# Optimization experiments

Measured on AMD Instinct MI355X. Metric: run time of the kernel, lower is better.

## Reference

```python
import jax, jax.numpy as jnp
import numpy as np

N, D, H, E = 4096, 512, 8, 131072
DH = D // H
BN_EPS = 1e-5


def setup_inputs() -> dict:
    key = jax.random.key(0)
    ks = jax.random.split(key, 12)
    def w(k, shape):
        return jax.random.normal(k, shape, dtype=jnp.float32) * 0.02
    return {
        'x': jax.random.normal(ks[0], (N, D), dtype=jnp.float32),
        'edge_index': jax.random.randint(ks[1], (2, E), 0, N),
        'edge_attr': jax.random.normal(ks[2], (E, D), dtype=jnp.float32),
        # GINE MLP: Linear(D,D) -> ReLU -> Linear(D,D)  (torch layout [out,in])
        'w_gin1': w(ks[3], (D, D)), 'b_gin1': jnp.zeros((D,), jnp.float32),
        'w_gin2': w(ks[4], (D, D)), 'b_gin2': jnp.zeros((D,), jnp.float32),
        # MultiheadAttention in/out projections
        'w_qkv': w(ks[5], (3 * D, D)), 'b_qkv': jnp.zeros((3 * D,), jnp.float32),
        'w_o': w(ks[6], (D, D)), 'b_o': jnp.zeros((D,), jnp.float32),
        # BatchNorm affine params
        'bn1l_g': jnp.ones((D,), jnp.float32), 'bn1l_b': jnp.zeros((D,), jnp.float32),
        'bn1a_g': jnp.ones((D,), jnp.float32), 'bn1a_b': jnp.zeros((D,), jnp.float32),
        # FFN: D -> 2D -> D
        'w_ff1': w(ks[7], (2 * D, D)), 'b_ff1': jnp.zeros((2 * D,), jnp.float32),
        'w_ff2': w(ks[8], (D, 2 * D)), 'b_ff2': jnp.zeros((D,), jnp.float32),
        'bn2_g': jnp.ones((D,), jnp.float32), 'bn2_b': jnp.zeros((D,), jnp.float32),
    }


def _bn(x, g, b):
    # BatchNorm1d in training mode: batch statistics over the node dim
    m = jnp.mean(x, axis=0)
    v = jnp.var(x, axis=0)
    return (x - m) * jax.lax.rsqrt(v + BN_EPS) * g + b


def _forward(x, edge_index, edge_attr,
             w_gin1, b_gin1, w_gin2, b_gin2,
             w_qkv, b_qkv, w_o, b_o,
             bn1l_g, bn1l_b, bn1a_g, bn1a_b,
             w_ff1, b_ff1, w_ff2, b_ff2, bn2_g, bn2_b):
    h_in = x
    src, dst = edge_index[0], edge_index[1]
    # --- local GINEConv: nn((1+eps)*x + sum_j relu(x_j + e_ji)), eps=0 ---
    msg = jax.nn.relu(x[src] + edge_attr)                       # [E, D]
    agg = jax.ops.segment_sum(msg, dst, num_segments=N)         # [N, D]
    gin_h = x + agg
    h_local = jax.nn.relu(gin_h @ w_gin1.T + b_gin1) @ w_gin2.T + b_gin2
    h_local = _bn(h_in + h_local, bn1l_g, bn1l_b)               # residual + BN
    # --- global multi-head self-attention over all nodes (single graph) ---
    qkv = x @ w_qkv.T + b_qkv                                   # [N, 3D]
    q, k, v = jnp.split(qkv, 3, axis=-1)
    q = q.reshape(N, H, DH).transpose(1, 0, 2)                  # [H, N, DH]
    k = k.reshape(N, H, DH).transpose(1, 0, 2)
    v = v.reshape(N, H, DH).transpose(1, 0, 2)
    scores = jnp.einsum('hnd,hmd->hnm', q, k) / np.float32(np.sqrt(DH))
    attn = jax.nn.softmax(scores, axis=-1)                      # [H, N, N]
    o = jnp.einsum('hnm,hmd->hnd', attn, v).transpose(1, 0, 2).reshape(N, D)
    h_attn = _bn(h_in + (o @ w_o.T + b_o), bn1a_g, bn1a_b)
    # --- combine branches + FFN block ---
    h = h_local + h_attn
    h = h + (jax.nn.relu(h @ w_ff1.T + b_ff1) @ w_ff2.T + b_ff2)
    return _bn(h, bn2_g, bn2_b)


def reference(x, edge_index, edge_attr,
              w_gin1, b_gin1, w_gin2, b_gin2,
              w_qkv, b_qkv, w_o, b_o,
              bn1l_g, bn1l_b, bn1a_g, bn1a_b,
              w_ff1, b_ff1, w_ff2, b_ff2, bn2_g, bn2_b):
    return _forward(x, edge_index, edge_attr,
                    w_gin1, b_gin1, w_gin2, b_gin2,
                    w_qkv, b_qkv, w_o, b_o,
                    bn1l_g, bn1l_b, bn1a_g, bn1a_b,
                    w_ff1, b_ff1, w_ff2, b_ff2, bn2_g, bn2_b)
```

## Files before the change

### kernel.cpp

```cpp
#include <hip/hip_runtime.h>

#define Nn 4096
#define Dd 512
#define Hh 8
#define Ee 131072
#define DEGCAP 96

typedef __attribute__((ext_vector_type(8))) short short8v;
typedef __attribute__((ext_vector_type(8))) unsigned short ushort8v;
typedef __attribute__((ext_vector_type(4))) short short4v;
typedef __attribute__((ext_vector_type(4))) float f32x4v;
typedef __attribute__((ext_vector_type(4))) unsigned short ushort4v;

__device__ __forceinline__ float bf2f(unsigned short u) {
    return __uint_as_float(((unsigned int)u) << 16);
}
__device__ __forceinline__ unsigned short f2bf(float f) {
    unsigned int u = __float_as_uint(f);
    return (unsigned short)((u + 0x7fff + ((u >> 16) & 1)) >> 16);
}
__device__ __forceinline__ void gl_lds16(const void* g, void* l) {
    __builtin_amdgcn_global_load_lds((const __attribute__((address_space(1))) void*)g,
                                     (__attribute__((address_space(3))) void*)l, 16, 0, 0);
}

struct CastJobs {
    const float* src[6];
    unsigned short* dst[6];
    int start[7];
    int* cnt;
    float* stats;
};

__global__ __launch_bounds__(256) void cast_multi(CastJobs cj) {
    int gid = blockIdx.x * 256 + threadIdx.x;
    if (gid < 4096) cj.cnt[gid] = 0;
    if (gid < 6144) cj.stats[gid] = 0.f;
    int b = blockIdx.x;
    int j = 0;
    while (b >= cj.start[j + 1]) j++;
    int off = (b - cj.start[j]) * 1024 + threadIdx.x * 4;
    f32x4v v = *(const f32x4v*)(cj.src[j] + off);
    ushort4v o;
    o.x = f2bf(v.x); o.y = f2bf(v.y); o.z = f2bf(v.z); o.w = f2bf(v.w);
    *(ushort4v*)(cj.dst[j] + off) = o;
}

__global__ __launch_bounds__(256) void edge_scatter(const int* __restrict__ ei,
                                                    int* __restrict__ cnt,
                                                    int* __restrict__ eidx) {
    int e = blockIdx.x * 256 + threadIdx.x;
    int d = ei[Ee + e];
    int pos = atomicAdd(&cnt[d], 1);
    if (pos < DEGCAP) eidx[d * DEGCAP + pos] = e;
}

__global__ __launch_bounds__(256) void gine_gather(const float* __restrict__ x,
                                                   const int* __restrict__ ei,
                                                   const float* __restrict__ ea,
                                                   const int* __restrict__ cnt,
                                                   const int* __restrict__ eidx,
                                                   unsigned short* __restrict__ gh,
                                                   unsigned short* __restrict__ xb) {
    __shared__ int se[DEGCAP];
    __shared__ int ss[DEGCAP];
    __shared__ float part[512];
    const int node = blockIdx.x;
    const int t = threadIdx.x;
    const int deg = min(cnt[node], DEGCAP);
    const int tc = t & 127, ep = t >> 7;

    if (t < deg) {
        int e = eidx[node * DEGCAP + t];
        se[t] = e;
        ss[t] = ei[e];
    }
    __syncthreads();

    f32x4v acc = {0.f, 0.f, 0.f, 0.f};
    int k = ep;
    while (k + 2 < deg) {
        int e0 = se[k], s0 = ss[k];
        int e1 = se[k + 2], s1 = ss[k + 2];
        f32x4v ev0 = *(const f32x4v*)(ea + (size_t)e0 * Dd + tc * 4);
        f32x4v xv0 = *(const f32x4v*)(x + (size_t)s0 * Dd + tc * 4);
        f32x4v ev1 = *(const f32x4v*)(ea + (size_t)e1 * Dd + tc * 4);
        f32x4v xv1 = *(const f32x4v*)(x + (size_t)s1 * Dd + tc * 4);
#pragma unroll
        for (int i = 0; i < 4; i++) {
            acc[i] += fmaxf(xv0[i] + ev0[i], 0.f);
            acc[i] += fmaxf(xv1[i] + ev1[i], 0.f);
        }
        k += 4;
    }
    if (k < deg) {
        int e0 = se[k], s0 = ss[k];
        f32x4v ev0 = *(const f32x4v*)(ea + (size_t)e0 * Dd + tc * 4);
        f32x4v xv0 = *(const f32x4v*)(x + (size_t)s0 * Dd + tc * 4);
#pragma unroll
        for (int i = 0; i < 4; i++) acc[i] += fmaxf(xv0[i] + ev0[i], 0.f);
    }

    if (ep) *(f32x4v*)&part[tc * 4] = acc;
    __syncthreads();
    if (!ep) {
        f32x4v o = *(const f32x4v*)&part[tc * 4];
        f32x4v xd = *(const f32x4v*)(x + (size_t)node * Dd + tc * 4);
        ushort4v ov, xv;
#pragma unroll
        for (int i = 0; i < 4; i++) {
            ov[i] = f2bf(xd[i] + acc[i] + o[i]);
            xv[i] = f2bf(xd[i]);
        }
        *(ushort4v*)(gh + (size_t)node * Dd + tc * 4) = ov;
        *(ushort4v*)(xb + (size_t)node * Dd + tc * 4) = xv;
    }
}

template <int K, int MB, bool RELU, bool OUTBF16, bool ADDRES, bool SXADD, int SOFF, bool ACOMB>
__device__ __forceinline__ void gemm_body(char* smem,
                                          const short* __restrict__ A,
                                          const short* __restrict__ B,
                                          const float* __restrict__ bias,
                                          const float* __restrict__ res,
                                          void* __restrict__ outp, int Nc,
                                          const float* __restrict__ sx,
                                          float* __restrict__ stats,
                                          const unsigned short* __restrict__ op0,
                                          const unsigned short* __restrict__ op1,
                                          const float* __restrict__ lsum,
                                          int bx, int by, int t) {
    constexpr int BM = MB * 32;
    short* lA = (short*)smem;
    short* lB = (short*)(smem + MB * 2048);
    float* sst = (float*)(smem + MB * 2048 + 8192);
    const int lane = t & 63, w = t >> 6;
    const int wr = w >> 1, wc = w & 1;
    const int l15 = lane & 15, lhi = lane >> 4;
    const int m0 = by * BM, n0 = bx * 128;
    f32x4v acc[MB][4] = {};
    const int c0 = t, c1 = t + 256;

    for (int k0 = 0; k0 < K; k0 += 32) {
        __syncthreads();
        if constexpr (ACOMB) {
            int r = c0 >> 2, s = c0 & 3;
            int row = m0 + r;
            int kb = k0 + s * 8;
            int h = k0 >> 6;
            float inv = 1.f / (lsum[(size_t)h * Nn + row] + lsum[(size_t)(Hh + h) * Nn + row]);
            ushort8v p0 = *(const ushort8v*)&op0[(size_t)row * 512 + kb];
            ushort8v p1 = *(const ushort8v*)&op1[(size_t)row * 512 + kb];
            short8v ov;
#pragma unroll
            for (int i = 0; i < 8; i++) ov[i] = (short)f2bf((bf2f(p0[i]) + bf2f(p1[i])) * inv);
            *(short8v*)((char*)lA + c0 * 16) = ov;
        } else {
            gl_lds16(A + (size_t)(m0 + (c0 >> 2)) * K + k0 + (c0 & 3) * 8, (char*)lA + c0 * 16);
            if constexpr (MB == 4)
                gl_lds16(A + (size_t)(m0 + (c1 >> 2)) * K + k0 + (c1 & 3) * 8, (char*)lA + c1 * 16);
        }
        gl_lds16(B + (size_t)(n0 + (c0 >> 2)) * K + k0 + (c0 & 3) * 8, (char*)lB + c0 * 16);
        gl_lds16(B + (size_t)(n0 + (c1 >> 2)) * K + k0 + (c1 & 3) * 8, (char*)lB + c1 * 16);
        __syncthreads();
        short8v af[MB], bf[4];
#pragma unroll
        for (int m = 0; m < MB; m++)
            af[m] = *(const short8v*)&lA[(wr * (MB * 16) + m * 16 + l15) * 32 + lhi * 8];
#pragma unroll
        for (int n = 0; n < 4; n++)
            bf[n] = *(const short8v*)&lB[(wc * 64 + n * 16 + l15) * 32 + lhi * 8];
#pragma unroll
        for (int m = 0; m < MB; m++)
#pragma unroll
            for (int n = 0; n < 4; n++)
                acc[m][n] = __builtin_amdgcn_mfma_f32_16x16x32_bf16(af[m], bf[n], acc[m][n], 0, 0, 0);
    }

    float csum[4] = {0.f, 0.f, 0.f, 0.f}, cssq[4] = {0.f, 0.f, 0.f, 0.f};

#pragma unroll
    for (int m = 0; m < MB; m++)
#pragma unroll
        for (int n = 0; n < 4; n++)
#pragma unroll
            for (int j = 0; j < 4; j++) {
                int col = n0 + wc * 64 + n * 16 + l15;
                int row = m0 + wr * (MB * 16) + m * 16 + lhi * 4 + j;
                size_t idx = (size_t)row * Nc + col;
                float v = acc[m][n][j] + bias[col];
                if (RELU) v = fmaxf(v, 0.f);
                if (ADDRES) v += res[idx];
                if constexpr (SOFF >= 0) {
                    float a = SXADD ? (sx[idx] + v) : v;
                    csum[n] += a;
                    cssq[n] += a * a;
                }
                if (OUTBF16)
                    ((unsigned short*)outp)[idx] = f2bf(v);
                else
                    ((float*)outp)[idx] = v;
            }

    if constexpr (SOFF >= 0) {
        sst[t] = 0.f;
        __syncthreads();
#pragma unroll
        for (int n = 0; n < 4; n++) {
            float s = csum[n], q = cssq[n];
            s += __shfl_xor(s, 16); s += __shfl_xor(s, 32);
            q += __shfl_xor(q, 16); q += __shfl_xor(q, 32);
            if (lhi == 0) {
                int c = wc * 64 + n * 16 + l15;
                atomicAdd(&sst[c * 2], s);
                atomicAdd(&sst[c * 2 + 1], q);
            }
        }
        __syncthreads();
        atomicAdd(&stats[SOFF + (t & 1) * 512 + n0 + (t >> 1)], sst[t]);
    }
}

__device__ __forceinline__ void attn_body(char* smem, const short* __restrict__ qkv,
                                          unsigned short* __restrict__ opart0,
                                          unsigned short* __restrict__ opart1,
                                          float* __restrict__ lsum,
                                          int bx, int by, int t) {
    const int lane = t & 63, w = t >> 6;
    const int h = by >> 1, half = by & 1;
    const int kvbase = half * 2048;
    const int qw = bx * 128 + w * 32;
    const int l15 = lane & 15, lhi = lane >> 4;
    const int ksw = l15 & 7;
    const int qs3 = (l15 >> 1) & 7;
    unsigned short* __restrict__ opart = half ? opart1 : opart0;

    short* pP = (short*)(smem + 32768) + w * 2048;

    short8v qf[2][2];
#pragma unroll
    for (int g = 0; g < 2; g++)
#pragma unroll
        for (int kk = 0; kk < 2; kk++)
            qf[g][kk] = *(const short8v*)&qkv[(size_t)(qw + g * 16 + l15) * 1536 + h * 64 + kk * 32 + lhi * 8];

    f32x4v oacc[2][4] = {};
    float lrow[2] = {0.f, 0.f};
    const float SC2 = 0.125f * 1.44269504f;

    int kidx[4][2];
#pragma unroll
    for (int r = 0; r < 4; r++)
#pragma unroll
        for (int kk = 0; kk < 2; kk++)
            kidx[r][kk] = (l15 + r * 16) * 64 + (((kk * 4 + lhi) ^ ksw) * 8);

    int pw_idx[4], prd_idx[2];
#pragma unroll
    for (int c2 = 0; c2 < 4; c2++)
        pw_idx[c2] = l15 * 64 + (((c2 * 2 + (lhi >> 1)) ^ qs3) * 8) + ((lhi & 1) * 4);
#pragma unroll
    for (int c = 0; c < 2; c++)
        prd_idx[c] = l15 * 64 + (((c * 4 + lhi) ^ qs3) * 8);

    unsigned vbase0 = (unsigned)(size_t)(smem + 16384) + lhi * 256 + l15 * 2;

    auto stage = [&](int kt, int b) {
        int kv0 = kvbase + kt * 64;
#pragma unroll
        for (int i = 0; i < 2; i++) {
            gl_lds16(qkv + (size_t)(kv0 + (t >> 3) + 32 * i) * 1536 + 512 + h * 64 + ((t & 7) ^ ((t >> 3) & 7)) * 8,
                     smem + b * 8192 + t * 16 + i * 4096);
        }
#pragma unroll
        for (int i = 0; i < 2; i++) {
            int db = (t >> 7) + 2 * i;
            int kv = (t >> 1) & 63;
            int dh_in = (t & 1) * 8;
            gl_lds16(qkv + (size_t)(kv0 + kv) * 1536 + 1024 + h * 64 + db * 16 + dh_in,
                     smem + 16384 + b * 8192 + t * 16 + i * 4096);
        }
    };

    stage(0, 0);
    __syncthreads();

    for (int kt = 0; kt < 32; kt++) {
        const int b = kt & 1;
        if (kt + 1 < 32) stage(kt + 1, b ^ 1);

        const short* Kb = (const short*)smem + b * 4096;
        const unsigned vbase = vbase0 + b * 8192;

        f32x4v s0[4] = {}, s1[4] = {};
        __builtin_amdgcn_s_setprio(1);
#pragma unroll
        for (int r = 0; r < 4; r++) {
            short8v k0 = *(const short8v*)&Kb[kidx[r][0]];
            short8v k1 = *(const short8v*)&Kb[kidx[r][1]];
            s0[r] = __builtin_amdgcn_mfma_f32_16x16x32_bf16(k0, qf[0][0], s0[r], 0, 0, 0);
            s0[r] = __builtin_amdgcn_mfma_f32_16x16x32_bf16(k1, qf[0][1], s0[r], 0, 0, 0);
            s1[r] = __builtin_amdgcn_mfma_f32_16x16x32_bf16(k0, qf[1][0], s1[r], 0, 0, 0);
            s1[r] = __builtin_amdgcn_mfma_f32_16x16x32_bf16(k1, qf[1][1], s1[r], 0, 0, 0);
        }
        __builtin_amdgcn_s_setprio(0);

#pragma unroll
        for (int g = 0; g < 2; g++) {
            f32x4v* s = g ? s1 : s0;
            float p[16];
            float rs = 0.f;
#pragma unroll
            for (int r = 0; r < 4; r++)
#pragma unroll
                for (int j = 0; j < 4; j++) {
                    float e = exp2f(fmaf(s[r][j], SC2, -4.f));
                    p[r * 4 + j] = e;
                    rs += e;
                }
            rs += __shfl_xor(rs, 16);
            rs += __shfl_xor(rs, 32);
            lrow[g] += rs;

            short* pPg = pP + g * 1024;
#pragma unroll
            for (int c2 = 0; c2 < 4; c2++) {
                short4v pk;
#pragma unroll
                for (int j = 0; j < 4; j++) pk[j] = (short)f2bf(p[c2 * 4 + j]);
                *(short4v*)&pPg[pw_idx[c2]] = pk;
            }
        }
        asm volatile("" ::: "memory");

        short8v pf[2][2];
#pragma unroll
        for (int g = 0; g < 2; g++)
#pragma unroll
            for (int c = 0; c < 2; c++)
                pf[g][c] = *(const short8v*)&pP[g * 1024 + prd_idx[c]];

        short4v v00a, v00b, v01a, v01b, v10a, v10b, v11a, v11b;
        short4v v20a, v20b, v21a, v21b, v30a, v30b, v31a, v31b;
        asm volatile("ds_read_b64_tr_b16 %0, %1" : "=v"(v00a) : "v"(vbase));
        asm volatile("ds_read_b64_tr_b16 %0, %1 offset:128" : "=v"(v00b) : "v"(vbase));
        asm volatile("ds_read_b64_tr_b16 %0, %1 offset:1024" : "=v"(v01a) : "v"(vbase));
        asm volatile("ds_read_b64_tr_b16 %0, %1 offset:1152" : "=v"(v01b) : "v"(vbase));
        asm volatile("ds_read_b64_tr_b16 %0, %1 offset:2048" : "=v"(v10a) : "v"(vbase));
        asm volatile("ds_read_b64_tr_b16 %0, %1 offset:2176" : "=v"(v10b) : "v"(vbase));
        asm volatile("ds_read_b64_tr_b16 %0, %1 offset:3072" : "=v"(v11a) : "v"(vbase));
        asm volatile("ds_read_b64_tr_b16 %0, %1 offset:3200" : "=v"(v11b) : "v"(vbase));
        asm volatile("ds_read_b64_tr_b16 %0, %1 offset:4096" : "=v"(v20a) : "v"(vbase));
        asm volatile("ds_read_b64_tr_b16 %0, %1 offset:4224" : "=v"(v20b) : "v"(vbase));
        asm volatile("ds_read_b64_tr_b16 %0, %1 offset:5120" : "=v"(v21a) : "v"(vbase));
        asm volatile("ds_read_b64_tr_b16 %0, %1 offset:5248" : "=v"(v21b) : "v"(vbase));
        asm volatile("ds_read_b64_tr_b16 %0, %1 offset:6144" : "=v"(v30a) : "v"(vbase));
        asm volatile("ds_read_b64_tr_b16 %0, %1 offset:6272" : "=v"(v30b) : "v"(vbase));
        asm volatile("ds_read_b64_tr_b16 %0, %1 offset:7168" : "=v"(v31a) : "v"(vbase));
        asm volatile("ds_read_b64_tr_b16 %0, %1 offset:7296" : "=v"(v31b) : "v"(vbase));

        asm volatile("s_waitcnt lgkmcnt(0)" ::: "memory");
        __builtin_amdgcn_sched_barrier(0);

#define VFCAT(a, b) __builtin_shufflevector(a, b, 0, 1, 2, 3, 4, 5, 6, 7)
        short8v vv[4][2];
        vv[0][0] = VFCAT(v00a, v00b); vv[0][1] = VFCAT(v01a, v01b);
        vv[1][0] = VFCAT(v10a, v10b); vv[1][1] = VFCAT(v11a, v11b);
        vv[2][0] = VFCAT(v20a, v20b); vv[2][1] = VFCAT(v21a, v21b);
        vv[3][0] = VFCAT(v30a, v30b); vv[3][1] = VFCAT(v31a, v31b);
#undef VFCAT
        __builtin_amdgcn_s_setprio(1);
#pragma unroll
        for (int g = 0; g < 2; g++)
#pragma unroll
            for (int n = 0; n < 4; n++) {
                oacc[g][n] = __builtin_amdgcn_mfma_f32_16x16x32_bf16(pf[g][0], vv[n][0], oacc[g][n], 0, 0, 0);
                oacc[g][n] = __builtin_amdgcn_mfma_f32_16x16x32_bf16(pf[g][1], vv[n][1], oacc[g][n], 0, 0, 0);
            }
        __builtin_amdgcn_s_setprio(0);

        __syncthreads();
    }

#pragma unroll
    for (int g = 0; g < 2; g++) {
#pragma unroll
        for (int j = 0; j < 4; j++) {
            int row = qw + g * 16 + lhi * 4 + j;
#pragma unroll
            for (int n = 0; n < 4; n++)
                opart[(size_t)row * Dd + h * 64 + n * 16 + l15] = f2bf(oacc[g][n][j]);
        }
        if (lhi == 0)
            lsum[(size_t)(half * Hh + h) * Nn + qw + g * 16 + l15] = lrow[g];
    }
}

__global__ __launch_bounds__(256) void gin1_qkv(const short* ginh, const short* wg1b,
                                                const float* b_gin1, unsigned short* t1,
                                                const short* xb, const short* wqkvb,
                                                const float* b_qkv, unsigned short* qkvb) {
    __shared__ char smem[16384];
    int b = blockIdx.x, t = threadIdx.x;
    if (b < 256) {
        gemm_body<512, 2, true, true, false, false, -1, false>(
            smem, ginh, wg1b, b_gin1, nullptr, t1, 512, nullptr, nullptr,
            nullptr, nullptr, nullptr, b & 3, b >> 2, t);
    } else {
        int bb = b - 256;
        gemm_body<512, 4, false, true, false, false, -1, false>(
            smem, xb, wqkvb, b_qkv, nullptr, qkvb, 1536, nullptr, nullptr,
            nullptr, nullptr, nullptr, bb % 12, bb / 12, t);
    }
}

__global__ __launch_bounds__(256) void gin2_attn(const short* qkvb, unsigned short* op0,
                                                 unsigned short* op1, float* lsum,
                                                 const short* t1, const short* wg2b,
                                                 const float* b_gin2, float* hlp,
                                                 const float* x, float* stats) {
    __shared__ char smem[49152];
    int b = blockIdx.x, t = threadIdx.x;
    if (b < 512) {
        attn_body(smem, qkvb, op0, op1, lsum, b & 31, b >> 5, t);
    } else {
        int bb = b - 512;
        gemm_body<512, 2, false, false, false, true, 0, false>(
            smem, t1, wg2b, b_gin2, nullptr, hlp, 512, x, stats,
            nullptr, nullptr, nullptr, bb & 3, bb >> 2, t);
    }
}

__global__ __launch_bounds__(256) void oproj_fused(const short* wob, const float* b_o,
                                                   float* attn_pre, const float* x, float* stats,
                                                   const unsigned short* op0,
                                                   const unsigned short* op1,
                                                   const float* lsum) {
    __shared__ char smem[13312];
    gemm_body<512, 2, false, false, false, true, 1024, true>(
        smem, nullptr, wob, b_o, nullptr, attn_pre, 512, x, stats,
        op0, op1, lsum, blockIdx.x, blockIdx.y, threadIdx.x);
}

__global__ __launch_bounds__(256) void ff1_k(const short* hb, const short* wf1b,
                                             const float* b_ff1, unsigned short* t2) {
    __shared__ char smem[16384];
    gemm_body<512, 4, true, true, false, false, -1, false>(
        smem, hb, wf1b, b_ff1, nullptr, t2, 1024, nullptr, nullptr,
        nullptr, nullptr, nullptr, blockIdx.x, blockIdx.y, threadIdx.x);
}

__global__ __launch_bounds__(256) void ff2_k(const short* t2, const short* wf2b,
                                             const float* b_ff2, const float* hbuf,
                                             float* dout, float* stats) {
    __shared__ char smem[13312];
    gemm_body<1024, 2, false, false, true, false, 4096, false>(
        smem, t2, wf2b, b_ff2, hbuf, dout, 512, nullptr, stats,
        nullptr, nullptr, nullptr, blockIdx.x, blockIdx.y, threadIdx.x);
}

__global__ __launch_bounds__(256) void bn_combine(const float* __restrict__ x,
                                                  const float* __restrict__ p1,
                                                  const float* __restrict__ p2,
                                                  const float* __restrict__ stats,
                                                  const float* __restrict__ g1,
                                                  const float* __restrict__ b1,
                                                  const float* __restrict__ g2,
                                                  const float* __restrict__ b2,
                                                  float* __restrict__ h,
                                                  unsigned short* __restrict__ hb) {
    int i0 = (blockIdx.x * 256 + threadIdx.x) * 4;
    int c0 = i0 & 511;
    f32x4v xv = *(const f32x4v*)(x + i0);
    f32x4v av = *(const f32x4v*)(p1 + i0);
    f32x4v bv = *(const f32x4v*)(p2 + i0);
    f32x4v hv;
    ushort4v hbv;
#pragma unroll
    for (int e = 0; e < 4; e++) {
        int c = c0 + e;
        float ma = stats[c] * (1.f / Nn);
        float va = stats[512 + c] * (1.f / Nn) - ma * ma;
        float sA = g1[c] * rsqrtf(va + 1e-5f);
        float bA = b1[c] - ma * sA;
        float mb = stats[1024 + c] * (1.f / Nn);
        float vb = stats[1536 + c] * (1.f / Nn) - mb * mb;
        float sB = g2[c] * rsqrtf(vb + 1e-5f);
        float bB = b2[c] - mb * sB;
        float a = xv[e] + av[e];
        float b = xv[e] + bv[e];
        float val = a * sA + bA + b * sB + bB;
        hv[e] = val;
        hbv[e] = f2bf(val);
    }
    *(f32x4v*)(h + i0) = hv;
    *(ushort4v*)(hb + i0) = hbv;
}

__global__ __launch_bounds__(256) void bn_apply(float* __restrict__ out,
                                                const float* __restrict__ stats,
                                                const float* __restrict__ g,
                                                const float* __restrict__ b) {
    int i0 = (blockIdx.x * 256 + threadIdx.x) * 4;
    int c0 = i0 & 511;
    f32x4v v = *(const f32x4v*)(out + i0);
#pragma unroll
    for (int e = 0; e < 4; e++) {
        int c = c0 + e;
        float m = stats[4096 + c] * (1.f / Nn);
        float va = stats[4608 + c] * (1.f / Nn) - m * m;
        float s = g[c] * rsqrtf(va + 1e-5f);
        v[e] = (v[e] - m) * s + b[c];
    }
    *(f32x4v*)(out + i0) = v;
}

extern "C" void kernel_launch(void* const* d_in, const int* in_sizes, int n_in,
                              void* d_out, int out_size, void* d_ws, size_t ws_size,
                              hipStream_t stream) {
    const float* x = (const float*)d_in[0];
    const int* ei = (const int*)d_in[1];
    const float* ea = (const float*)d_in[2];
    const float* w_gin1 = (const float*)d_in[3];
    const float* b_gin1 = (const float*)d_in[4];
    const float* w_gin2 = (const float*)d_in[5];
    const float* b_gin2 = (const float*)d_in[6];
    const float* w_qkv = (const float*)d_in[7];
    const float* b_qkv = (const float*)d_in[8];
    const float* w_o = (const float*)d_in[9];
    const float* b_o = (const float*)d_in[10];
    const float* bn1l_g = (const float*)d_in[11];
    const float* bn1l_b = (const float*)d_in[12];
    const float* bn1a_g = (const float*)d_in[13];
    const float* bn1a_b = (const float*)d_in[14];
    const float* w_ff1 = (const float*)d_in[15];
    const float* b_ff1 = (const float*)d_in[16];
    const float* w_ff2 = (const float*)d_in[17];
    const float* b_ff2 = (const float*)d_in[18];
    const float* bn2_g = (const float*)d_in[19];
    const float* bn2_b = (const float*)d_in[20];

    char* ws = (char*)d_ws;
    unsigned short* wg1b = (unsigned short*)(ws + 0);
    unsigned short* wg2b = (unsigned short*)(ws + 524288);
    unsigned short* wqkvb = (unsigned short*)(ws + 1048576);
    unsigned short* wob = (unsigned short*)(ws + 2621440);
    unsigned short* wf1b = (unsigned short*)(ws + 3145728);
    unsigned short* wf2b = (unsigned short*)(ws + 4194304);
    unsigned short* xb = (unsigned short*)(ws + 5242880);
    unsigned short* qkvb = (unsigned short*)(ws + 9437184);
    int* eidx = (int*)(ws + 22020096);
    int* cnt = (int*)(ws + 23592960);
    unsigned short* ginh = (unsigned short*)(ws + 30408704);
    float* lsum = (float*)(ws + 30408704);
    unsigned short* t1 = (unsigned short*)(ws + 34603008);
    float* hlp = (float*)(ws + 38797312);
    float* attn_pre = (float*)(ws + 51380224);
    float* hbuf = (float*)(ws + 59768832);
    unsigned short* opart0 = (unsigned short*)(ws + 59768832);
    unsigned short* hb = (unsigned short*)(ws + 68157440);
    unsigned short* t2 = (unsigned short*)(ws + 72351744);
    unsigned short* opart1 = (unsigned short*)(ws + 72351744);
    float* stats = (float*)(ws + 80740352);

    CastJobs cj;
    cj.src[0] = w_gin1; cj.dst[0] = wg1b;
    cj.src[1] = w_gin2; cj.dst[1] = wg2b;
    cj.src[2] = w_qkv;  cj.dst[2] = wqkvb;
    cj.src[3] = w_o;    cj.dst[3] = wob;
    cj.src[4] = w_ff1;  cj.dst[4] = wf1b;
    cj.src[5] = w_ff2;  cj.dst[5] = wf2b;
    cj.cnt = cnt;
    cj.stats = stats;
    int nelem[6] = {Dd * Dd, Dd * Dd, 3 * Dd * Dd, Dd * Dd, 2 * Dd * Dd, 2 * Dd * Dd};
    cj.start[0] = 0;
    for (int i = 0; i < 6; i++) cj.start[i + 1] = cj.start[i] + nelem[i] / 1024;
    cast_multi<<<cj.start[6], 256, 0, stream>>>(cj);

    edge_scatter<<<Ee / 256, 256, 0, stream>>>(ei, cnt, eidx);
    gine_gather<<<Nn, 256, 0, stream>>>(x, ei, ea, cnt, eidx, ginh, xb);

    gin1_qkv<<<640, 256, 0, stream>>>((const short*)ginh, (const short*)wg1b, b_gin1, t1,
                                      (const short*)xb, (const short*)wqkvb, b_qkv, qkvb);

    gin2_attn<<<768, 256, 0, stream>>>((const short*)qkvb, opart0, opart1, lsum,
                                       (const short*)t1, (const short*)wg2b, b_gin2, hlp,
                                       x, stats);

    oproj_fused<<<dim3(4, 64), 256, 0, stream>>>((const short*)wob, b_o, attn_pre, x, stats,
                                                 opart0, opart1, lsum);

    bn_combine<<<Nn * Dd / 1024, 256, 0, stream>>>(x, hlp, attn_pre, stats,
                                                   bn1l_g, bn1l_b, bn1a_g, bn1a_b, hbuf, hb);

    ff1_k<<<dim3(8, 32), 256, 0, stream>>>((const short*)hb, (const short*)wf1b, b_ff1, t2);
    ff2_k<<<dim3(4, 64), 256, 0, stream>>>((const short*)t2, (const short*)wf2b, b_ff2,
                                           hbuf, (float*)d_out, stats);

    bn_apply<<<Nn * Dd / 1024, 256, 0, stream>>>((float*)d_out, stats, bn2_g, bn2_b);
}
```

Measured before the change: 260.6 us.

## Split attention KV into quarters with 64 queries per wave; use bf16 FFN residual

The attention work is reorganised: each block now covers 256 queries (64 per wave) against one quarter of the keys, so every K/V tile loaded into shared memory is reused by twice as many queries. Four partial outputs and four partial row sums are combined in the o-projection prologue, and shared memory grows to 64KB with launch bounds of two blocks per CU. Separately, bn_combine no longer writes an fp32 copy of h, and ff2 adds the bf16 hb as its residual, cutting memory traffic at a small precision cost. The larger per-wave register state for the accumulators may reduce occupancy or cause spills.

```diff
diff --git a/kernel.cpp b/kernel.cpp
--- a/kernel.cpp
+++ b/kernel.cpp
@@ -117,17 +117,19 @@
     }
 }
 
-template <int K, int MB, bool RELU, bool OUTBF16, bool ADDRES, bool SXADD, int SOFF, bool ACOMB>
+template <int K, int MB, bool RELU, bool OUTBF16, int RESMODE, bool SXADD, int SOFF, bool ACOMB>
 __device__ __forceinline__ void gemm_body(char* smem,
                                           const short* __restrict__ A,
                                           const short* __restrict__ B,
                                           const float* __restrict__ bias,
-                                          const float* __restrict__ res,
+                                          const void* __restrict__ res,
                                           void* __restrict__ outp, int Nc,
                                           const float* __restrict__ sx,
                                           float* __restrict__ stats,
                                           const unsigned short* __restrict__ op0,
                                           const unsigned short* __restrict__ op1,
+                                          const unsigned short* __restrict__ op2,
+                                          const unsigned short* __restrict__ op3,
                                           const float* __restrict__ lsum,
                                           int bx, int by, int t) {
     constexpr int BM = MB * 32;
@@ -148,12 +150,16 @@
             int row = m0 + r;
             int kb = k0 + s * 8;
             int h = k0 >> 6;
-            float inv = 1.f / (lsum[(size_t)h * Nn + row] + lsum[(size_t)(Hh + h) * Nn + row]);
+            float inv = 1.f / (lsum[(size_t)h * Nn + row] + lsum[(size_t)(Hh + h) * Nn + row] +
+                               lsum[(size_t)(2 * Hh + h) * Nn + row] + lsum[(size_t)(3 * Hh + h) * Nn + row]);
             ushort8v p0 = *(const ushort8v*)&op0[(size_t)row * 512 + kb];
             ushort8v p1 = *(const ushort8v*)&op1[(size_t)row * 512 + kb];
+            ushort8v p2 = *(const ushort8v*)&op2[(size_t)row * 512 + kb];
+            ushort8v p3 = *(const ushort8v*)&op3[(size_t)row * 512 + kb];
             short8v ov;
 #pragma unroll
-            for (int i = 0; i < 8; i++) ov[i] = (short)f2bf((bf2f(p0[i]) + bf2f(p1[i])) * inv);
+            for (int i = 0; i < 8; i++)
+                ov[i] = (short)f2bf((bf2f(p0[i]) + bf2f(p1[i]) + bf2f(p2[i]) + bf2f(p3[i])) * inv);
             *(short8v*)((char*)lA + c0 * 16) = ov;
         } else {
             gl_lds16(A + (size_t)(m0 + (c0 >> 2)) * K + k0 + (c0 & 3) * 8, (char*)lA + c0 * 16);
@@ -190,7 +196,8 @@
                 size_t idx = (size_t)row * Nc + col;
                 float v = acc[m][n][j] + bias[col];
                 if (RELU) v = fmaxf(v, 0.f);
-                if (ADDRES) v += res[idx];
+                if constexpr (RESMODE == 1) v += ((const float*)res)[idx];
+                if constexpr (RESMODE == 2) v += bf2f(((const unsigned short*)res)[idx]);
                 if constexpr (SOFF >= 0) {
                     float a = SXADD ? (sx[idx] + v) : v;
                     csum[n] += a;
@@ -222,30 +229,32 @@
 }
 
 __device__ __forceinline__ void attn_body(char* smem, const short* __restrict__ qkv,
-                                          unsigned short* __restrict__ opart0,
-                                          unsigned short* __restrict__ opart1,
+                                          unsigned short* __restrict__ op0,
+                                          unsigned short* __restrict__ op1,
+                                          unsigned short* __restrict__ op2,
+                                          unsigned short* __restrict__ op3,
                                           float* __restrict__ lsum,
                                           int bx, int by, int t) {
     const int lane = t & 63, w = t >> 6;
-    const int h = by >> 1, half = by & 1;
-    const int kvbase = half * 2048;
-    const int qw = bx * 128 + w * 32;
+    const int h = by >> 2, quarter = by & 3;
+    const int kvbase = quarter * 1024;
+    const int qw = bx * 256 + w * 64;
     const int l15 = lane & 15, lhi = lane >> 4;
     const int ksw = l15 & 7;
     const int qs3 = (l15 >> 1) & 7;
-    unsigned short* __restrict__ opart = half ? opart1 : opart0;
-
-    short* pP = (short*)(smem + 32768) + w * 2048;
-
-    short8v qf[2][2];
-#pragma unroll
-    for (int g = 0; g < 2; g++)
+    unsigned short* __restrict__ opart = quarter == 0 ? op0 : quarter == 1 ? op1 : quarter == 2 ? op2 : op3;
+
+    short* pP = (short*)(smem + 32768) + w * 4096;
+
+    short8v qf[4][2];
+#pragma unroll
+    for (int g = 0; g < 4; g++)
 #pragma unroll
         for (int kk = 0; kk < 2; kk++)
             qf[g][kk] = *(const short8v*)&qkv[(size_t)(qw + g * 16 + l15) * 1536 + h * 64 + kk * 32 + lhi * 8];
 
-    f32x4v oacc[2][4] = {};
-    float lrow[2] = {0.f, 0.f};
+    f32x4v oacc[4][4] = {};
+    float lrow[4] = {0.f, 0.f, 0.f, 0.f};
     const float SC2 = 0.125f * 1.44269504f;
 
     int kidx[4][2];
@@ -285,36 +294,36 @@
     stage(0, 0);
     __syncthreads();
 
-    for (int kt = 0; kt < 32; kt++) {
+    for (int kt = 0; kt < 16; kt++) {
         const int b = kt & 1;
-        if (kt + 1 < 32) stage(kt + 1, b ^ 1);
+        if (kt + 1 < 16) stage(kt + 1, b ^ 1);
 
         const short* Kb = (const short*)smem + b * 4096;
         const unsigned vbase = vbase0 + b * 8192;
 
-        f32x4v s0[4] = {}, s1[4] = {};
+        f32x4v s[4][4] = {};
         __builtin_amdgcn_s_setprio(1);
 #pragma unroll
         for (int r = 0; r < 4; r++) {
             short8v k0 = *(const short8v*)&Kb[kidx[r][0]];
             short8v k1 = *(const short8v*)&Kb[kidx[r][1]];
-            s0[r] = __builtin_amdgcn_mfma_f32_16x16x32_bf16(k0, qf[0][0], s0[r], 0, 0, 0);
-            s0[r] = __builtin_amdgcn_mfma_f32_16x16x32_bf16(k1, qf[0][1], s0[r], 0, 0, 0);
-            s1[r] = __builtin_amdgcn_mfma_f32_16x16x32_bf16(k0, qf[1][0], s1[r], 0, 0, 0);
-            s1[r] = __builtin_amdgcn_mfma_f32_16x16x32_bf16(k1, qf[1][1], s1[r], 0, 0, 0);
+#pragma unroll
+            for (int g = 0; g < 4; g++) {
+                s[g][r] = __builtin_amdgcn_mfma_f32_16x16x32_bf16(k0, qf[g][0], s[g][r], 0, 0, 0);
+                s[g][r] = __builtin_amdgcn_mfma_f32_16x16x32_bf16(k1, qf[g][1], s[g][r], 0, 0, 0);
+            }
         }
         __builtin_amdgcn_s_setprio(0);
 
 #pragma unroll
-        for (int g = 0; g < 2; g++) {
-            f32x4v* s = g ? s1 : s0;
+        for (int g = 0; g < 4; g++) {
             float p[16];
             float rs = 0.f;
 #pragma unroll
             for (int r = 0; r < 4; r++)
 #pragma unroll
                 for (int j = 0; j < 4; j++) {
-                    float e = exp2f(fmaf(s[r][j], SC2, -4.f));
+                    float e = exp2f(fmaf(s[g][r][j], SC2, -4.f));
                     p[r * 4 + j] = e;
                     rs += e;
                 }
@@ -333,9 +342,9 @@
         }
         asm volatile("" ::: "memory");
 
-        short8v pf[2][2];
-#pragma unroll
-        for (int g = 0; g < 2; g++)
+        short8v pf[4][2];
+#pragma unroll
+        for (int g = 0; g < 4; g++)
 #pragma unroll
             for (int c = 0; c < 2; c++)
                 pf[g][c] = *(const short8v*)&pP[g * 1024 + prd_idx[c]];
@@ -371,7 +380,7 @@
 #undef VFCAT
         __builtin_amdgcn_s_setprio(1);
 #pragma unroll
-        for (int g = 0; g < 2; g++)
+        for (int g = 0; g < 4; g++)
 #pragma unroll
             for (int n = 0; n < 4; n++) {
                 oacc[g][n] = __builtin_amdgcn_mfma_f32_16x16x32_bf16(pf[g][0], vv[n][0], oacc[g][n], 0, 0, 0);
@@ -383,7 +392,7 @@
     }
 
 #pragma unroll
-    for (int g = 0; g < 2; g++) {
+    for (int g = 0; g < 4; g++) {
 #pragma unroll
         for (int j = 0; j < 4; j++) {
             int row = qw + g * 16 + lhi * 4 + j;
@@ -392,7 +401,7 @@
                 opart[(size_t)row * Dd + h * 64 + n * 16 + l15] = f2bf(oacc[g][n][j]);
         }
         if (lhi == 0)
-            lsum[(size_t)(half * Hh + h) * Nn + qw + g * 16 + l15] = lrow[g];
+            lsum[(size_t)(quarter * Hh + h) * Nn + qw + g * 16 + l15] = lrow[g];
     }
 }
 
@@ -403,31 +412,32 @@
     __shared__ char smem[16384];
     int b = blockIdx.x, t = threadIdx.x;
     if (b < 256) {
-        gemm_body<512, 2, true, true, false, false, -1, false>(
+        gemm_body<512, 2, true, true, 0, false, -1, false>(
             smem, ginh, wg1b, b_gin1, nullptr, t1, 512, nullptr, nullptr,
-            nullptr, nullptr, nullptr, b & 3, b >> 2, t);
+            nullptr, nullptr, nullptr, nullptr, nullptr, b & 3, b >> 2, t);
     } else {
         int bb = b - 256;
-        gemm_body<512, 4, false, true, false, false, -1, false>(
+        gemm_body<512, 4, false, true, 0, false, -1, false>(
             smem, xb, wqkvb, b_qkv, nullptr, qkvb, 1536, nullptr, nullptr,
-            nullptr, nullptr, nullptr, bb % 12, bb / 12, t);
-    }
-}
-
-__global__ __launch_bounds__(256) void gin2_attn(const short* qkvb, unsigned short* op0,
-                                                 unsigned short* op1, float* lsum,
-                                                 const short* t1, const short* wg2b,
-                                                 const float* b_gin2, float* hlp,
-                                                 const float* x, float* stats) {
-    __shared__ char smem[49152];
+            nullptr, nullptr, nullptr, nullptr, nullptr, bb % 12, bb / 12, t);
+    }
+}
+
+__global__ __launch_bounds__(256, 2) void gin2_attn(const short* qkvb, unsigned short* op0,
+                                                    unsigned short* op1, unsigned short* op2,
+                                                    unsigned short* op3, float* lsum,
+                                                    const short* t1, const short* wg2b,
+                                                    const float* b_gin2, float* hlp,
+                                                    const float* x, float* stats) {
+    __shared__ char smem[65536];
     int b = blockIdx.x, t = threadIdx.x;
     if (b < 512) {
-        attn_body(smem, qkvb, op0, op1, lsum, b & 31, b >> 5, t);
+        attn_body(smem, qkvb, op0, op1, op2, op3, lsum, b & 15, b >> 4, t);
     } else {
         int bb = b - 512;
-        gemm_body<512, 2, false, false, false, true, 0, false>(
+        gemm_body<512, 2, false, false, 0, true, 0, false>(
             smem, t1, wg2b, b_gin2, nullptr, hlp, 512, x, stats,
-            nullptr, nullptr, nullptr, bb & 3, bb >> 2, t);
+            nullptr, nullptr, nullptr, nullptr, nullptr, bb & 3, bb >> 2, t);
     }
 }
 
@@ -435,28 +445,30 @@
                                                    float* attn_pre, const float* x, float* stats,
                                                    const unsigned short* op0,
                                                    const unsigned short* op1,
+                                                   const unsigned short* op2,
+                                                   const unsigned short* op3,
                                                    const float* lsum) {
     __shared__ char smem[13312];
-    gemm_body<512, 2, false, false, false, true, 1024, true>(
+    gemm_body<512, 2, false, false, 0, true, 1024, true>(
         smem, nullptr, wob, b_o, nullptr, attn_pre, 512, x, stats,
-        op0, op1, lsum, blockIdx.x, blockIdx.y, threadIdx.x);
+        op0, op1, op2, op3, lsum, blockIdx.x, blockIdx.y, threadIdx.x);
 }
 
 __global__ __launch_bounds__(256) void ff1_k(const short* hb, const short* wf1b,
                                              const float* b_ff1, unsigned short* t2) {
     __shared__ char smem[16384];
-    gemm_body<512, 4, true, true, false, false, -1, false>(
+    gemm_body<512, 4, true, true, 0, false, -1, false>(
         smem, hb, wf1b, b_ff1, nullptr, t2, 1024, nullptr, nullptr,
-        nullptr, nullptr, nullptr, blockIdx.x, blockIdx.y, threadIdx.x);
+        nullptr, nullptr, nullptr, nullptr, nullptr, blockIdx.x, blockIdx.y, threadIdx.x);
 }
 
 __global__ __launch_bounds__(256) void ff2_k(const short* t2, const short* wf2b,
-                                             const float* b_ff2, const float* hbuf,
+                                             const float* b_ff2, const unsigned short* hb,
                                              float* dout, float* stats) {
     __shared__ char smem[13312];
-    gemm_body<1024, 2, false, false, true, false, 4096, false>(
-        smem, t2, wf2b, b_ff2, hbuf, dout, 512, nullptr, stats,
-        nullptr, nullptr, nullptr, blockIdx.x, blockIdx.y, threadIdx.x);
+    gemm_body<1024, 2, false, false, 2, false, 4096, false>(
+        smem, t2, wf2b, b_ff2, hb, dout, 512, nullptr, stats,
+        nullptr, nullptr, nullptr, nullptr, nullptr, blockIdx.x, blockIdx.y, threadIdx.x);
 }
 
 __global__ __launch_bounds__(256) void bn_combine(const float* __restrict__ x,
@@ -467,14 +479,12 @@
                                                   const float* __restrict__ b1,
                                                   const float* __restrict__ g2,
                                                   const float* __restrict__ b2,
-                                                  float* __restrict__ h,
                                                   unsigned short* __restrict__ hb) {
     int i0 = (blockIdx.x * 256 + threadIdx.x) * 4;
     int c0 = i0 & 511;
     f32x4v xv = *(const f32x4v*)(x + i0);
     f32x4v av = *(const f32x4v*)(p1 + i0);
     f32x4v bv = *(const f32x4v*)(p2 + i0);
-    f32x4v hv;
     ushort4v hbv;
 #pragma unroll
     for (int e = 0; e < 4; e++) {
@@ -489,11 +499,8 @@
         float bB = b2[c] - mb * sB;
         float a = xv[e] + av[e];
         float b = xv[e] + bv[e];
-        float val = a * sA + bA + b * sB + bB;
-        hv[e] = val;
-        hbv[e] = f2bf(val);
-    }
-    *(f32x4v*)(h + i0) = hv;
+        hbv[e] = f2bf(a * sA + bA + b * sB + bB);
+    }
     *(ushort4v*)(hb + i0) = hbv;
 }
 
@@ -555,10 +562,11 @@
     float* lsum = (float*)(ws + 30408704);
     unsigned short* t1 = (unsigned short*)(ws + 34603008);
     float* hlp = (float*)(ws + 38797312);
+    unsigned short* opart2 = (unsigned short*)(ws + 47185920);
     float* attn_pre = (float*)(ws + 51380224);
-    float* hbuf = (float*)(ws + 59768832);
     unsigned short* opart0 = (unsigned short*)(ws + 59768832);
     unsigned short* hb = (unsigned short*)(ws + 68157440);
+    unsigned short* opart3 = (unsigned short*)(ws + 68157440);
     unsigned short* t2 = (unsigned short*)(ws + 72351744);
     unsigned short* opart1 = (unsigned short*)(ws + 72351744);
     float* stats = (float*)(ws + 80740352);
@@ -583,19 +591,19 @@
     gin1_qkv<<<640, 256, 0, stream>>>((const short*)ginh, (const short*)wg1b, b_gin1, t1,
                                       (const short*)xb, (const short*)wqkvb, b_qkv, qkvb);
 
-    gin2_attn<<<768, 256, 0, stream>>>((const short*)qkvb, opart0, opart1, lsum,
+    gin2_attn<<<768, 256, 0, stream>>>((const short*)qkvb, opart0, opart1, opart2, opart3, lsum,
                                        (const short*)t1, (const short*)wg2b, b_gin2, hlp,
                                        x, stats);
 
     oproj_fused<<<dim3(4, 64), 256, 0, stream>>>((const short*)wob, b_o, attn_pre, x, stats,
-                                                 opart0, opart1, lsum);
+                                                 opart0, opart1, opart2, opart3, lsum);
 
     bn_combine<<<Nn * Dd / 1024, 256, 0, stream>>>(x, hlp, attn_pre, stats,
-                                                   bn1l_g, bn1l_b, bn1a_g, bn1a_b, hbuf, hb);
+                                                   bn1l_g, bn1l_b, bn1a_g, bn1a_b, hb);
 
     ff1_k<<<dim3(8, 32), 256, 0, stream>>>((const short*)hb, (const short*)wf1b, b_ff1, t2);
     ff2_k<<<dim3(4, 64), 256, 0, stream>>>((const short*)t2, (const short*)wf2b, b_ff2,
-                                           hbuf, (float*)d_out, stats);
+                                           hb, (float*)d_out, stats);
 
     bn_apply<<<Nn * Dd / 1024, 256, 0, stream>>>((float*)d_out, stats, bn2_g, bn2_b);
 }
```

After: 257.2 us, median of 2. About the same (-1.3%).
